# Optimization experiments

Measured on AMD Instinct MI355X. Metric: run time of the kernel, lower is better.

The kernel has to match this reference:

```python
import jax, jax.numpy as jnp
import numpy as np


def setup_inputs() -> dict:
    key = jax.random.key(0)
    k1, k2, k3, k4 = jax.random.split(key, 4)
    B, N, D, L = 4, 512, 256, 64
    x = jax.random.normal(k1, (B, N, D), dtype=jnp.float32)
    adj = jax.random.uniform(k2, (B, N, N), dtype=jnp.float32)
    W_proj = jax.random.normal(k3, (L, D), dtype=jnp.float32) * (1.0 / np.sqrt(D))
    learn_w = jax.random.uniform(k4, (L,), dtype=jnp.float32)  # init.uniform_(0,1)
    return {"x": x, "adj": adj, "W_proj": W_proj, "learn_w": learn_w}


def reference(x, adj, W_proj, learn_w):
    # x: [B,N,D]; projection (no bias): x_hat [B,N,L]
    x_hat = jnp.einsum('bnd,ld->bnl', x, W_proj)
    # pairwise L1-style abs difference: [B,N,N,L]
    diff = jnp.abs(x_hat[:, :, None, :] - x_hat[:, None, :, :])
    # weighted reduce over feature dim: [B,N,N]
    dist = jnp.einsum('bijl,l->bij', diff, learn_w)
    out = jax.nn.leaky_relu(dist, negative_slope=0.01)
    out = out - jnp.max(out, axis=-1, keepdims=True)
    soft_adj = adj * jnp.exp(out)
    # NOTE: faithful to original: epsilon added AFTER the division
    soft_adj = soft_adj / jnp.sum(soft_adj, axis=-1, keepdims=True) + 1e-10
    return soft_adj
```

## Files before the change

kernel.cpp:

```cpp
#include <hip/hip_runtime.h>
#include <math.h>

#define BB 4
#define NN 512
#define DD 256
#define LL 64

#define K1_NR 4
#define WST  260
#define IPB  8

__global__ __launch_bounds__(256) void k1_proj(const float* __restrict__ x,
                                               const float* __restrict__ Wp,
                                               const float* __restrict__ lw,
                                               float* __restrict__ xhatT) {
  __shared__ __align__(16) float Wl[LL * WST];
  __shared__ __align__(16) float xs[K1_NR * DD];
  const int bx = blockIdx.x;
  const int b  = bx >> 7;
  const int n0 = (bx & 127) * K1_NR;
  const int t  = threadIdx.x;
  const int l  = t & 63;
  const int r  = t >> 6;

  const float4* Wp4 = (const float4*)Wp;
  #pragma unroll
  for (int it = 0; it < 16; ++it) {
    int idx = it * 256 + t;
    int ll  = idx >> 6;
    int dq  = idx & 63;
    float4 wv = Wp4[idx];
    float  w  = lw[ll];
    wv.x *= w; wv.y *= w; wv.z *= w; wv.w *= w;
    *(float4*)&Wl[ll * WST + dq * 4] = wv;
  }
  ((float4*)xs)[t] = ((const float4*)x)[((size_t)(b * NN + n0)) * (DD / 4) + t];
  __syncthreads();

  const float4* xrow = (const float4*)&xs[r * DD];
  const float4* wrow = (const float4*)&Wl[l * WST];
  float4 a = make_float4(0.f, 0.f, 0.f, 0.f);
  #pragma unroll 8
  for (int dd = 0; dd < 64; ++dd) {
    float4 xv = xrow[dd];
    float4 wv = wrow[dd];
    a.x += xv.x * wv.x;
    a.y += xv.y * wv.y;
    a.z += xv.z * wv.z;
    a.w += xv.w * wv.w;
  }
  xhatT[(size_t)b * (LL * NN) + (size_t)l * NN + (n0 + r)] = (a.x + a.y) + (a.z + a.w);
}

__global__ __launch_bounds__(512) void k2_main(const float* __restrict__ xhatT,
                                               const float* __restrict__ adj,
                                               float* __restrict__ out) {
  __shared__ __align__(16) float xj_s[LL * NN];
  __shared__ __align__(16) float xi_s[LL * IPB];
  __shared__ float redm[IPB * 8];
  __shared__ float reds[IPB * 8];

  const int bx   = blockIdx.x;
  const int b    = bx >> 6;
  const int i0   = (bx & 63) * IPB;
  const int t    = threadIdx.x;
  const int wave = t >> 6;
  const int lane = t & 63;

  const float* xb = xhatT + (size_t)b * (LL * NN);

  const float* adjb = adj + ((size_t)b * NN + i0) * NN;
  float adjv[IPB];
  #pragma unroll
  for (int r = 0; r < IPB; ++r) adjv[r] = adjb[(size_t)r * NN + t];

  {
    const float4* xb4 = (const float4*)xb;
    float4* xj4 = (float4*)xj_s;
    #pragma unroll
    for (int it = 0; it < 16; ++it)
      xj4[it * 512 + t] = xb4[it * 512 + t];
  }
  {
    int l = t >> 3, r = t & 7;
    xi_s[t] = xb[l * NN + i0 + r];
  }
  __syncthreads();

  float acc[IPB] = {0.f, 0.f, 0.f, 0.f, 0.f, 0.f, 0.f, 0.f};
  const float4* xi4 = (const float4*)xi_s;
  #pragma unroll 16
  for (int l = 0; l < LL; ++l) {
    float  p  = xj_s[l * NN + t];
    float4 a0 = xi4[l * 2 + 0];
    float4 a1 = xi4[l * 2 + 1];
    acc[0] += fabsf(a0.x - p);
    acc[1] += fabsf(a0.y - p);
    acc[2] += fabsf(a0.z - p);
    acc[3] += fabsf(a0.w - p);
    acc[4] += fabsf(a1.x - p);
    acc[5] += fabsf(a1.y - p);
    acc[6] += fabsf(a1.z - p);
    acc[7] += fabsf(a1.w - p);
  }

  #pragma unroll
  for (int r = 0; r < IPB; ++r) {
    float d = acc[r];
    acc[r] = d >= 0.f ? d : 0.01f * d;
  }

  #pragma unroll
  for (int r = 0; r < IPB; ++r) {
    float m = acc[r];
    #pragma unroll
    for (int off = 32; off > 0; off >>= 1)
      m = fmaxf(m, __shfl_xor(m, off, 64));
    if (lane == 0) redm[r * 8 + wave] = m;
  }
  __syncthreads();

  float e[IPB];
  #pragma unroll
  for (int r = 0; r < IPB; ++r) {
    float m = redm[r * 8 + 0];
    #pragma unroll
    for (int k = 1; k < 8; ++k) m = fmaxf(m, redm[r * 8 + k]);
    e[r] = adjv[r] * __expf(acc[r] - m);
  }

  #pragma unroll
  for (int r = 0; r < IPB; ++r) {
    float s = e[r];
    #pragma unroll
    for (int off = 32; off > 0; off >>= 1)
      s += __shfl_xor(s, off, 64);
    if (lane == 0) reds[r * 8 + wave] = s;
  }
  __syncthreads();

  float* outb = out + ((size_t)b * NN + i0) * NN;
  #pragma unroll
  for (int r = 0; r < IPB; ++r) {
    float s = reds[r * 8 + 0];
    #pragma unroll
    for (int k = 1; k < 8; ++k) s += reds[r * 8 + k];
    outb[(size_t)r * NN + t] = e[r] / s + 1e-10f;
  }
}

extern "C" void kernel_launch(void* const* d_in, const int* in_sizes, int n_in,
                              void* d_out, int out_size, void* d_ws, size_t ws_size,
                              hipStream_t stream) {
  const float* x   = (const float*)d_in[0];
  const float* adj = (const float*)d_in[1];
  const float* Wp  = (const float*)d_in[2];
  const float* lw  = (const float*)d_in[3];
  float* out   = (float*)d_out;
  float* xhatT = (float*)d_ws;

  hipLaunchKernelGGL(k1_proj, dim3(BB * NN / K1_NR), dim3(256), 0, stream,
                     x, Wp, lw, xhatT);
  hipLaunchKernelGGL(k2_main, dim3(BB * NN / IPB), dim3(512), 0, stream,
                     xhatT, adj, out);
}
```

Baseline: 80.45 us.

## Fuse projection and softmax kernels into one cooperative kernel with grid sync

Result: slower. 170.4 us (+111.8%).

```diff
diff --git a/kernel.cpp b/kernel.cpp
--- a/kernel.cpp
+++ b/kernel.cpp
@@ -1,99 +1,97 @@
 #include <hip/hip_runtime.h>
+#include <hip/hip_cooperative_groups.h>
 #include <math.h>
 
 #define BB 4
 #define NN 512
 #define DD 256
 #define LL 64
+#define IPB 8
+#define WST 260
+#define GRID (BB * NN / IPB)
 
-#define K1_NR 4
-#define WST  260
-#define IPB  8
+namespace cg = cooperative_groups;
 
-__global__ __launch_bounds__(256) void k1_proj(const float* __restrict__ x,
-                                               const float* __restrict__ Wp,
-                                               const float* __restrict__ lw,
-                                               float* __restrict__ xhatT) {
-  __shared__ __align__(16) float Wl[LL * WST];
-  __shared__ __align__(16) float xs[K1_NR * DD];
-  const int bx = blockIdx.x;
-  const int b  = bx >> 7;
-  const int n0 = (bx & 127) * K1_NR;
-  const int t  = threadIdx.x;
-  const int l  = t & 63;
-  const int r  = t >> 6;
-
-  const float4* Wp4 = (const float4*)Wp;
-  #pragma unroll
-  for (int it = 0; it < 16; ++it) {
-    int idx = it * 256 + t;
-    int ll  = idx >> 6;
-    int dq  = idx & 63;
-    float4 wv = Wp4[idx];
-    float  w  = lw[ll];
-    wv.x *= w; wv.y *= w; wv.z *= w; wv.w *= w;
-    *(float4*)&Wl[ll * WST + dq * 4] = wv;
-  }
-  ((float4*)xs)[t] = ((const float4*)x)[((size_t)(b * NN + n0)) * (DD / 4) + t];
-  __syncthreads();
-
-  const float4* xrow = (const float4*)&xs[r * DD];
-  const float4* wrow = (const float4*)&Wl[l * WST];
-  float4 a = make_float4(0.f, 0.f, 0.f, 0.f);
-  #pragma unroll 8
-  for (int dd = 0; dd < 64; ++dd) {
-    float4 xv = xrow[dd];
-    float4 wv = wrow[dd];
-    a.x += xv.x * wv.x;
-    a.y += xv.y * wv.y;
-    a.z += xv.z * wv.z;
-    a.w += xv.w * wv.w;
-  }
-  xhatT[(size_t)b * (LL * NN) + (size_t)l * NN + (n0 + r)] = (a.x + a.y) + (a.z + a.w);
-}
-
-__global__ __launch_bounds__(512) void k2_main(const float* __restrict__ xhatT,
-                                               const float* __restrict__ adj,
-                                               float* __restrict__ out) {
-  __shared__ __align__(16) float xj_s[LL * NN];
+__global__ __launch_bounds__(512, 2) void fused(const float* __restrict__ x,
+                                                const float* __restrict__ adj,
+                                                const float* __restrict__ Wp,
+                                                const float* __restrict__ lw,
+                                                float* __restrict__ out) {
+  __shared__ __align__(16) float smem[LL * NN];
   __shared__ __align__(16) float xi_s[LL * IPB];
   __shared__ float redm[IPB * 8];
   __shared__ float reds[IPB * 8];
 
+  float* Wl = smem;
+  float* xs = smem + LL * WST;
+  float* xj = smem;
+
   const int bx   = blockIdx.x;
   const int b    = bx >> 6;
-  const int i0   = (bx & 63) * IPB;
+  const int n0   = (bx & 63) * IPB;
   const int t    = threadIdx.x;
   const int wave = t >> 6;
   const int lane = t & 63;
 
-  const float* xb = xhatT + (size_t)b * (LL * NN);
+  float* scr = out + (BB * NN * NN - BB * LL * NN);
 
-  const float* adjb = adj + ((size_t)b * NN + i0) * NN;
+  const float* adjb = adj + ((size_t)b * NN + n0) * NN;
   float adjv[IPB];
   #pragma unroll
   for (int r = 0; r < IPB; ++r) adjv[r] = adjb[(size_t)r * NN + t];
 
+  const float4* Wp4 = (const float4*)Wp;
+  #pragma unroll
+  for (int it = 0; it < 8; ++it) {
+    int idx = it * 512 + t;
+    int ll  = idx >> 6;
+    int dq  = idx & 63;
+    *(float4*)&Wl[ll * WST + dq * 4] = Wp4[idx];
+  }
   {
-    const float4* xb4 = (const float4*)xb;
-    float4* xj4 = (float4*)xj_s;
+    const float4* x4 = (const float4*)(x + ((size_t)b * NN + n0) * DD);
+    *(float4*)&xs[wave * WST + lane * 4] = x4[wave * 64 + lane];
+  }
+  __syncthreads();
+
+  {
+    const int l = t >> 3;
+    const int r = t & 7;
+    const float4* wrow = (const float4*)&Wl[l * WST];
+    const float4* xrow = (const float4*)&xs[r * WST];
+    float4 a = make_float4(0.f, 0.f, 0.f, 0.f);
+    #pragma unroll 8
+    for (int dd = 0; dd < 64; ++dd) {
+      float4 wv = wrow[dd];
+      float4 xv = xrow[dd];
+      a.x += xv.x * wv.x;
+      a.y += xv.y * wv.y;
+      a.z += xv.z * wv.z;
+      a.w += xv.w * wv.w;
+    }
+    float val = lw[l] * ((a.x + a.y) + (a.z + a.w));
+    xi_s[t] = val;
+    scr[(size_t)b * (LL * NN) + l * NN + (n0 + r)] = val;
+  }
+  __threadfence();
+  cg::this_grid().sync();
+
+  {
+    const float4* s4 = (const float4*)(scr + (size_t)b * (LL * NN));
+    float4* d4 = (float4*)xj;
     #pragma unroll
     for (int it = 0; it < 16; ++it)
-      xj4[it * 512 + t] = xb4[it * 512 + t];
-  }
-  {
-    int l = t >> 3, r = t & 7;
-    xi_s[t] = xb[l * NN + i0 + r];
+      d4[it * 512 + t] = s4[it * 512 + t];
   }
   __syncthreads();
 
   float acc[IPB] = {0.f, 0.f, 0.f, 0.f, 0.f, 0.f, 0.f, 0.f};
   const float4* xi4 = (const float4*)xi_s;
   #pragma unroll 16
-  for (int l = 0; l < LL; ++l) {
-    float  p  = xj_s[l * NN + t];
-    float4 a0 = xi4[l * 2 + 0];
-    float4 a1 = xi4[l * 2 + 1];
+  for (int l2 = 0; l2 < LL; ++l2) {
+    float  p  = xj[l2 * NN + t];
+    float4 a0 = xi4[l2 * 2 + 0];
+    float4 a1 = xi4[l2 * 2 + 1];
     acc[0] += fabsf(a0.x - p);
     acc[1] += fabsf(a0.y - p);
     acc[2] += fabsf(a0.z - p);
@@ -103,7 +101,6 @@
     acc[6] += fabsf(a1.z - p);
     acc[7] += fabsf(a1.w - p);
   }
-
   #pragma unroll
   for (int r = 0; r < IPB; ++r) {
     float d = acc[r];
@@ -139,14 +136,21 @@
   }
   __syncthreads();
 
-  float* outb = out + ((size_t)b * NN + i0) * NN;
+  float sden[IPB];
   #pragma unroll
   for (int r = 0; r < IPB; ++r) {
     float s = reds[r * 8 + 0];
     #pragma unroll
     for (int k = 1; k < 8; ++k) s += reds[r * 8 + k];
-    outb[(size_t)r * NN + t] = e[r] / s + 1e-10f;
+    sden[r] = s;
   }
+
+  cg::this_grid().sync();
+
+  float* outb = out + ((size_t)b * NN + n0) * NN;
+  #pragma unroll
+  for (int r = 0; r < IPB; ++r)
+    outb[(size_t)r * NN + t] = e[r] / sden[r] + 1e-10f;
 }
 
 extern "C" void kernel_launch(void* const* d_in, const int* in_sizes, int n_in,
@@ -156,11 +160,8 @@
   const float* adj = (const float*)d_in[1];
   const float* Wp  = (const float*)d_in[2];
   const float* lw  = (const float*)d_in[3];
-  float* out   = (float*)d_out;
-  float* xhatT = (float*)d_ws;
+  float* out = (float*)d_out;
 
-  hipLaunchKernelGGL(k1_proj, dim3(BB * NN / K1_NR), dim3(256), 0, stream,
-                     x, Wp, lw, xhatT);
-  hipLaunchKernelGGL(k2_main, dim3(BB * NN / IPB), dim3(512), 0, stream,
-                     xhatT, adj, out);
+  void* args[] = {(void*)&x, (void*)&adj, (void*)&Wp, (void*)&lw, (void*)&out};
+  hipLaunchCooperativeKernel((void*)fused, dim3(GRID), dim3(512), args, 0, stream);
 }
```
